# Optimization experiments

Hardware: AMD Instinct MI355X
Metric: run time of the kernel (lower is better)

## Reference

```python
import jax, jax.numpy as jnp
import numpy as np

MAX_REL = 64  # max_relative_position (init kwarg)


def setup_inputs() -> dict:
    B, S, D, K = 8, 2048, 256, MAX_REL
    key = jax.random.key(0)
    ks = jax.random.split(key, 12)
    scale = 0.02
    return {
        "repre": jax.random.normal(ks[0], (B, S, D), jnp.float32),
        "mask": jnp.ones((B, S), jnp.int32),
        "wq1": jax.random.normal(ks[1], (D, D), jnp.float32) * scale,
        "bq1": jnp.zeros((D,), jnp.float32),
        "wk1": jax.random.normal(ks[2], (D, D), jnp.float32) * scale,
        "bk1": jnp.zeros((D,), jnp.float32),
        "rel1": jax.random.normal(ks[3], (2 * K + 1, D), jnp.float32) * scale,
        "wq2": jax.random.normal(ks[4], (D, D), jnp.float32) * scale,
        "bq2": jnp.zeros((D,), jnp.float32),
        "wk2": jax.random.normal(ks[5], (D, D), jnp.float32) * scale,
        "bk2": jnp.zeros((D,), jnp.float32),
        "rel2": jax.random.normal(ks[6], (2 * K + 1, D), jnp.float32) * scale,
    }


def _attn_logits(x, wq, bq, wk, bk, rel_emb, invalid, rel_idx):
    # Single-head relative-position attention scores (OpenNMT style):
    # query is pre-scaled by 1/sqrt(d); relative-key bias folded into scores.
    B, S, D = x.shape
    q = (x @ wq.T + bq) / jnp.sqrt(jnp.asarray(D, x.dtype))  # [B,S,D]
    k = x @ wk.T + bk                                        # [B,S,D]
    scores = jnp.einsum("bqd,bkd->bqk", q, k)               # [B,S,S]
    # relative-position term: q . rel_emb[clip(k-q)] without the [S,S,D] table
    q_rel = jnp.einsum("bqd,rd->bqr", q, rel_emb)            # [B,S,2K+1]
    idx = jnp.broadcast_to(rel_idx[None, :, :], (B, S, S))
    rel_scores = jnp.take_along_axis(q_rel, idx, axis=2)     # [B,S,S]
    scores = scores + rel_scores
    return jnp.where(invalid, jnp.asarray(-1e18, scores.dtype), scores)


def reference(repre, mask, wq1, bq1, wk1, bk1, rel1, wq2, bq2, wk2, bk2, rel2):
    B, S, D = repre.shape
    K = MAX_REL
    pos = jnp.arange(S)
    rel_idx = jnp.clip(pos[None, :] - pos[:, None], -K, K) + K  # [S,S] in [0,2K]
    # square_mask = ~(mask^T @ mask): attend only where both positions valid
    invalid = (mask[:, :, None] * mask[:, None, :]) == 0        # [B,S,S] bool
    span_st_logits = _attn_logits(repre, wq1, bq1, wk1, bk1, rel1, invalid, rel_idx)
    span_ed_logits = _attn_logits(repre, wq2, bq2, wk2, bk2, rel2, invalid, rel_idx)
    return (span_st_logits, span_ed_logits)
```

## Files before the change

### kernel.cpp

```cpp
#include <hip/hip_runtime.h>
#include <hip/hip_bf16.h>

typedef __attribute__((ext_vector_type(4))) float f32x4;
typedef __attribute__((ext_vector_type(8))) short short8;

struct bf16x4 { __hip_bfloat16 a, b, c, d; };

#define BS   8
#define SQ   2048
#define DD   256
#define KREL 64
#define NREL 129

static const size_t OFF_XBF   = 0;
static const size_t OFF_WBF   = 8388608;
static const size_t OFF_RELBF = 8912896;
static const size_t OFF_WR    = 9044992;
static const size_t OFF_CR    = 9307136;
static const size_t OFF_QK    = 9309184;
static const size_t OFF_QR    = 42863616;

struct ConvArgs {
  const float* src[7];
  __hip_bfloat16* dst[7];
  float scale[7];
  int cum4[8];
};
struct bf4 { __hip_bfloat16 a, b, c, d; };

__global__ __launch_bounds__(256) void convert_k(ConvArgs A) {
  const int idx = blockIdx.x * 256 + threadIdx.x;
  if (idx >= A.cum4[7]) return;
  int rg = 0;
  #pragma unroll
  for (int t = 1; t < 7; ++t) rg += (idx >= A.cum4[t]);
  const int local = idx - A.cum4[rg];
  const float4 v = ((const float4*)A.src[rg])[local];
  const float sc = A.scale[rg];
  bf4 o;
  o.a = __float2bfloat16(v.x * sc);
  o.b = __float2bfloat16(v.y * sc);
  o.c = __float2bfloat16(v.z * sc);
  o.d = __float2bfloat16(v.w * sc);
  ((bf4*)A.dst[rg])[local] = o;
}

__global__ __launch_bounds__(256) void wr_k(const __hip_bfloat16* __restrict__ relbf,
                                            const __hip_bfloat16* __restrict__ wbf,
                                            const float* __restrict__ bq1,
                                            const float* __restrict__ bq2,
                                            __hip_bfloat16* __restrict__ wr,
                                            float* __restrict__ cr) {
  const int r = blockIdx.x;
  const int h = blockIdx.y;
  const int e = threadIdx.x;
  const int lane = e & 63, wv = e >> 6;
  const __hip_bfloat16* rel = relbf + (size_t)h * (NREL * DD);
  const __hip_bfloat16* wq  = wbf + (size_t)h * (2 * DD * DD);
  float a0 = 0.f, a1 = 0.f, a2 = 0.f, a3 = 0.f;
  if (r < NREL) {
    #pragma unroll 4
    for (int d = 0; d < DD; d += 4) {
      a0 += __bfloat162float(rel[r * DD + d + 0]) * __bfloat162float(wq[(d + 0) * DD + e]);
      a1 += __bfloat162float(rel[r * DD + d + 1]) * __bfloat162float(wq[(d + 1) * DD + e]);
      a2 += __bfloat162float(rel[r * DD + d + 2]) * __bfloat162float(wq[(d + 2) * DD + e]);
      a3 += __bfloat162float(rel[r * DD + d + 3]) * __bfloat162float(wq[(d + 3) * DD + e]);
    }
  }
  wr[((size_t)h * DD + r) * DD + e] = __float2bfloat16((a0 + a1) + (a2 + a3));

  const float* bq = h ? bq2 : bq1;
  float p = (r < NREL) ? bq[e] * 0.0625f * __bfloat162float(rel[r * DD + e]) : 0.f;
  #pragma unroll
  for (int o = 32; o > 0; o >>= 1) p += __shfl_down(p, o, 64);
  __shared__ float wred[4];
  if (lane == 0) wred[wv] = p;
  __syncthreads();
  if (e == 0) cr[h * DD + r] = (wred[0] + wred[1]) + (wred[2] + wred[3]);
}

__device__ __forceinline__ void stage_tile(const __hip_bfloat16* __restrict__ A,
                                           const __hip_bfloat16* __restrict__ B,
                                           int rowBase, int colBase, int k0,
                                           char* As, char* Bs, int wv, int lane) {
  #pragma unroll
  for (int inst = 0; inst < 2; ++inst) {
    const int lds_off = wv * 2048 + inst * 1024;
    const int e0 = (lds_off >> 1) + lane * 8;
    const int r  = e0 >> 5;
    const int kk = e0 & 31;
    __builtin_amdgcn_global_load_lds(
        (const __attribute__((address_space(1))) void*)(A + (size_t)(rowBase + r) * DD + k0 + kk),
        (__attribute__((address_space(3))) void*)(As + lds_off), 16, 0, 0);
    __builtin_amdgcn_global_load_lds(
        (const __attribute__((address_space(1))) void*)(B + (size_t)(colBase + r) * DD + k0 + kk),
        (__attribute__((address_space(3))) void*)(Bs + lds_off), 16, 0, 0);
  }
}

__device__ __forceinline__ void gemm_dbuf(const __hip_bfloat16* __restrict__ A,
                                          const __hip_bfloat16* __restrict__ B,
                                          int rowBase, int colBase,
                                          char* lds,
                                          f32x4 acc[4][4]) {
  const int tid  = threadIdx.x;
  const int lane = tid & 63;
  const int wv   = tid >> 6;
  const int wrow = (wv >> 1) * 64;
  const int wcol = (wv & 1) * 64;
  const int m    = lane & 15;
  const int quad = lane >> 4;

  char* As[2] = {lds, lds + 16384};
  char* Bs[2] = {lds + 8192, lds + 24576};

  const f32x4 zf = {0.f, 0.f, 0.f, 0.f};
  #pragma unroll
  for (int si = 0; si < 4; ++si)
    #pragma unroll
    for (int sj = 0; sj < 4; ++sj) acc[si][sj] = zf;

  stage_tile(A, B, rowBase, colBase, 0, As[0], Bs[0], wv, lane);
  __syncthreads();

  #pragma unroll
  for (int k = 0; k < 8; ++k) {
    const int cur = k & 1, nxt = cur ^ 1;
    if (k < 7)
      stage_tile(A, B, rowBase, colBase, (k + 1) * 32, As[nxt], Bs[nxt], wv, lane);

    short8 af[4], bf[4];
    #pragma unroll
    for (int s = 0; s < 4; ++s) {
      af[s] = *(const short8*)(As[cur] + (wrow + s * 16 + m) * 64 + quad * 16);
      bf[s] = *(const short8*)(Bs[cur] + (wcol + s * 16 + m) * 64 + quad * 16);
    }
    #pragma unroll
    for (int si = 0; si < 4; ++si)
      #pragma unroll
      for (int sj = 0; sj < 4; ++sj)
        acc[si][sj] = __builtin_amdgcn_mfma_f32_16x16x32_bf16(bf[sj], af[si], acc[si][sj], 0, 0, 0);
    __syncthreads();
  }
}

struct QKArgs {
  const __hip_bfloat16* X;
  const __hip_bfloat16* W[6];
  const float* bias[6];
  void* out[6];
  float bscale[6];
  int isf32[6];
};

__global__ __launch_bounds__(256) void qk_k(QKArgs A) {
  __shared__ char lds[32768];
  const int flat = blockIdx.x + (blockIdx.y << 1) + (blockIdx.z << 8);
  const int swz  = (flat & 7) * 192 + (flat >> 3);
  const int colT = swz & 1;
  const int rowT = (swz >> 1) & 127;
  const int z    = swz >> 8;
  const int rowBase = rowT * 128;
  const int colBase = colT * 128;
  f32x4 acc[4][4];
  gemm_dbuf(A.X, A.W[z], rowBase, colBase, lds, acc);

  const int tid  = threadIdx.x;
  const int lane = tid & 63;
  const int wv   = tid >> 6;
  const int wrow = (wv >> 1) * 64;
  const int wcol = (wv & 1) * 64;
  const int m    = lane & 15;
  const int quad = lane >> 4;

  const float* bias = A.bias[z];
  const float bs = A.bscale[z];
  const int f32o = A.isf32[z];
  float* fo = (float*)A.out[z];
  __hip_bfloat16* bo = (__hip_bfloat16*)A.out[z];

  #pragma unroll
  for (int si = 0; si < 4; ++si) {
    const int i = rowBase + wrow + si * 16 + m;
    #pragma unroll
    for (int sj = 0; sj < 4; ++sj) {
      const int j0 = colBase + wcol + sj * 16 + quad * 4;
      const f32x4 bj = *(const f32x4*)(bias + j0);
      f32x4 v;
      #pragma unroll
      for (int r = 0; r < 4; ++r) v[r] = acc[si][sj][r] + bj[r] * bs;
      const size_t idx = (size_t)i * DD + j0;
      if (f32o) {
        __builtin_nontemporal_store(v, (f32x4*)(fo + idx));
      } else {
        bf16x4 o;
        o.a = __float2bfloat16(v[0]);
        o.b = __float2bfloat16(v[1]);
        o.c = __float2bfloat16(v[2]);
        o.d = __float2bfloat16(v[3]);
        unsigned long long u;
        __builtin_memcpy(&u, &o, 8);
        __builtin_nontemporal_store(u, (unsigned long long*)(bo + idx));
      }
    }
  }
}

__global__ __launch_bounds__(256) void score_k(const __hip_bfloat16* __restrict__ Q1,
                                               const __hip_bfloat16* __restrict__ K1,
                                               const float* __restrict__ QR1,
                                               const __hip_bfloat16* __restrict__ Q2,
                                               const __hip_bfloat16* __restrict__ K2,
                                               const float* __restrict__ QR2,
                                               const int* __restrict__ mask,
                                               float* __restrict__ out) {
  __shared__ char lds[32768];
  const int flat = blockIdx.x + (blockIdx.y << 4) + (blockIdx.z << 8);
  const int swz  = ((flat & 7) << 9) | (flat >> 3);
  const int colT = swz & 15;
  const int rowT = (swz >> 4) & 15;
  const int z    = swz >> 8;
  const int h = z >> 3, b = z & 7;
  const __hip_bfloat16* Q  = (h ? Q2 : Q1) + (size_t)b * SQ * DD;
  const __hip_bfloat16* Kk = (h ? K2 : K1) + (size_t)b * SQ * DD;
  const float* QR = (h ? QR2 : QR1) + (size_t)b * SQ * DD;
  const int* mk = mask + b * SQ;
  float* outp = out + (size_t)z * SQ * SQ;
  const int rowBase = rowT * 128;
  const int colBase = colT * 128;

  f32x4 acc[4][4];
  gemm_dbuf(Q, Kk, rowBase, colBase, lds, acc);

  const int tid  = threadIdx.x;
  const int lane = tid & 63;
  const int wv   = tid >> 6;
  const int wrow = (wv >> 1) * 64;
  const int wcol = (wv & 1) * 64;
  const int m    = lane & 15;
  const int quad = lane >> 4;

  const int delta = colBase - rowBase;
  const int mode = (delta >= 192) ? 1 : (delta <= -192 ? -1 : 0);

  int4 mj4[4];
  #pragma unroll
  for (int sj = 0; sj < 4; ++sj)
    mj4[sj] = *(const int4*)(mk + colBase + wcol + sj * 16 + quad * 4);

  #pragma unroll
  for (int si = 0; si < 4; ++si) {
    const int i = rowBase + wrow + si * 16 + m;
    const int mi = mk[i];
    const float* qr_row = QR + (size_t)i * DD;
    float* orow = outp + (size_t)i * SQ;
    float relc = 0.f;
    if (mode) relc = qr_row[mode == 1 ? 2 * KREL : 0];
    #pragma unroll
    for (int sj = 0; sj < 4; ++sj) {
      const int j0 = colBase + wcol + sj * 16 + quad * 4;
      f32x4 v;
      if (mode) {
        #pragma unroll
        for (int r = 0; r < 4; ++r) v[r] = acc[si][sj][r] + relc;
      } else {
        #pragma unroll
        for (int r = 0; r < 4; ++r) {
          int d = j0 + r - i;
          d = d < -KREL ? -KREL : (d > KREL ? KREL : d);
          v[r] = acc[si][sj][r] + qr_row[d + KREL];
        }
      }
      const int4 mj = mj4[sj];
      if (!(mi && mj.x)) v[0] = -1e18f;
      if (!(mi && mj.y)) v[1] = -1e18f;
      if (!(mi && mj.z)) v[2] = -1e18f;
      if (!(mi && mj.w)) v[3] = -1e18f;
      __builtin_nontemporal_store(v, (f32x4*)(orow + j0));
    }
  }
}

extern "C" void kernel_launch(void* const* d_in, const int* in_sizes, int n_in,
                              void* d_out, int out_size, void* d_ws, size_t ws_size,
                              hipStream_t stream) {
  const float* repre = (const float*)d_in[0];
  const int*   mask  = (const int*)d_in[1];
  const float* wq1 = (const float*)d_in[2];
  const float* bq1 = (const float*)d_in[3];
  const float* wk1 = (const float*)d_in[4];
  const float* bk1 = (const float*)d_in[5];
  const float* rel1 = (const float*)d_in[6];
  const float* wq2 = (const float*)d_in[7];
  const float* bq2 = (const float*)d_in[8];
  const float* wk2 = (const float*)d_in[9];
  const float* bk2 = (const float*)d_in[10];
  const float* rel2 = (const float*)d_in[11];

  char* ws = (char*)d_ws;
  __hip_bfloat16* xbf   = (__hip_bfloat16*)(ws + OFF_XBF);
  __hip_bfloat16* wbf   = (__hip_bfloat16*)(ws + OFF_WBF);
  __hip_bfloat16* relbf = (__hip_bfloat16*)(ws + OFF_RELBF);
  __hip_bfloat16* wr    = (__hip_bfloat16*)(ws + OFF_WR);
  float*          cr    = (float*)(ws + OFF_CR);
  __hip_bfloat16* Q1 = (__hip_bfloat16*)(ws + OFF_QK);
  __hip_bfloat16* K1 = Q1 + (size_t)16384 * 256;
  __hip_bfloat16* Q2 = K1 + (size_t)16384 * 256;
  __hip_bfloat16* K2 = Q2 + (size_t)16384 * 256;
  float* QR1 = (float*)(ws + OFF_QR);
  float* QR2 = QR1 + (size_t)16384 * 256;

  ConvArgs ca;
  ca.src[0] = repre; ca.dst[0] = xbf;            ca.scale[0] = 1.f;
  ca.src[1] = wq1;   ca.dst[1] = wbf;            ca.scale[1] = 0.0625f;
  ca.src[2] = wk1;   ca.dst[2] = wbf + 65536;    ca.scale[2] = 1.f;
  ca.src[3] = wq2;   ca.dst[3] = wbf + 131072;   ca.scale[3] = 0.0625f;
  ca.src[4] = wk2;   ca.dst[4] = wbf + 196608;   ca.scale[4] = 1.f;
  ca.src[5] = rel1;  ca.dst[5] = relbf;          ca.scale[5] = 1.f;
  ca.src[6] = rel2;  ca.dst[6] = relbf + 33024;  ca.scale[6] = 1.f;
  const int sizes[7] = {4194304, 65536, 65536, 65536, 65536, 33024, 33024};
  int cum = 0;
  ca.cum4[0] = 0;
  for (int i = 0; i < 7; ++i) { cum += sizes[i] / 4; ca.cum4[i + 1] = cum; }
  const int nblk = (cum + 255) / 256;
  hipLaunchKernelGGL(convert_k, dim3(nblk), dim3(256), 0, stream, ca);

  hipLaunchKernelGGL(wr_k, dim3(256, 2), dim3(256), 0, stream, relbf, wbf, bq1, bq2, wr, cr);

  QKArgs qa;
  qa.X = xbf;
  qa.W[0] = wbf;          qa.bias[0] = bq1;      qa.bscale[0] = 0.0625f; qa.out[0] = Q1;  qa.isf32[0] = 0;
  qa.W[1] = wbf + 65536;  qa.bias[1] = bk1;      qa.bscale[1] = 1.f;     qa.out[1] = K1;  qa.isf32[1] = 0;
  qa.W[2] = wr;           qa.bias[2] = cr;       qa.bscale[2] = 1.f;     qa.out[2] = QR1; qa.isf32[2] = 1;
  qa.W[3] = wbf + 131072; qa.bias[3] = bq2;      qa.bscale[3] = 0.0625f; qa.out[3] = Q2;  qa.isf32[3] = 0;
  qa.W[4] = wbf + 196608; qa.bias[4] = bk2;      qa.bscale[4] = 1.f;     qa.out[4] = K2;  qa.isf32[4] = 0;
  qa.W[5] = wr + 65536;   qa.bias[5] = cr + 256; qa.bscale[5] = 1.f;     qa.out[5] = QR2; qa.isf32[5] = 1;
  hipLaunchKernelGGL(qk_k, dim3(2, 128, 6), dim3(256), 0, stream, qa);

  hipLaunchKernelGGL(score_k, dim3(16, 16, 16), dim3(256), 0, stream,
                     Q1, K1, QR1, Q2, K2, QR2, mask, (float*)d_out);
}
```

Before: 488.4 us.

## Triple-buffer GEMM K-loop with single barrier and use regular stores

```diff
diff --git a/kernel.cpp b/kernel.cpp
--- a/kernel.cpp
+++ b/kernel.cpp
@@ -98,7 +98,7 @@
   }
 }
 
-__device__ __forceinline__ void gemm_dbuf(const __hip_bfloat16* __restrict__ A,
+__device__ __forceinline__ void gemm_tbuf(const __hip_bfloat16* __restrict__ A,
                                           const __hip_bfloat16* __restrict__ B,
                                           int rowBase, int colBase,
                                           char* lds,
@@ -111,8 +111,8 @@
   const int m    = lane & 15;
   const int quad = lane >> 4;
 
-  char* As[2] = {lds, lds + 16384};
-  char* Bs[2] = {lds + 8192, lds + 24576};
+  char* As[3] = {lds,        lds + 16384, lds + 32768};
+  char* Bs[3] = {lds + 8192, lds + 24576, lds + 40960};
 
   const f32x4 zf = {0.f, 0.f, 0.f, 0.f};
   #pragma unroll
@@ -120,15 +120,21 @@
     #pragma unroll
     for (int sj = 0; sj < 4; ++sj) acc[si][sj] = zf;
 
-  stage_tile(A, B, rowBase, colBase, 0, As[0], Bs[0], wv, lane);
-  __syncthreads();
+  stage_tile(A, B, rowBase, colBase, 0,  As[0], Bs[0], wv, lane);
+  stage_tile(A, B, rowBase, colBase, 32, As[1], Bs[1], wv, lane);
 
   #pragma unroll
   for (int k = 0; k < 8; ++k) {
-    const int cur = k & 1, nxt = cur ^ 1;
-    if (k < 7)
-      stage_tile(A, B, rowBase, colBase, (k + 1) * 32, As[nxt], Bs[nxt], wv, lane);
-
+    if (k < 7) asm volatile("s_waitcnt vmcnt(4)" ::: "memory");
+    else       asm volatile("s_waitcnt vmcnt(0)" ::: "memory");
+    __builtin_amdgcn_sched_barrier(0);
+    __builtin_amdgcn_s_barrier();
+    __builtin_amdgcn_sched_barrier(0);
+    if (k < 6)
+      stage_tile(A, B, rowBase, colBase, (k + 2) * 32,
+                 As[(k + 2) % 3], Bs[(k + 2) % 3], wv, lane);
+
+    const int cur = k % 3;
     short8 af[4], bf[4];
     #pragma unroll
     for (int s = 0; s < 4; ++s) {
@@ -140,7 +146,6 @@
       #pragma unroll
       for (int sj = 0; sj < 4; ++sj)
         acc[si][sj] = __builtin_amdgcn_mfma_f32_16x16x32_bf16(bf[sj], af[si], acc[si][sj], 0, 0, 0);
-    __syncthreads();
   }
 }
 
@@ -154,7 +159,7 @@
 };
 
 __global__ __launch_bounds__(256) void qk_k(QKArgs A) {
-  __shared__ char lds[32768];
+  __shared__ char lds[49152];
   const int flat = blockIdx.x + (blockIdx.y << 1) + (blockIdx.z << 8);
   const int swz  = (flat & 7) * 192 + (flat >> 3);
   const int colT = swz & 1;
@@ -163,7 +168,7 @@
   const int rowBase = rowT * 128;
   const int colBase = colT * 128;
   f32x4 acc[4][4];
-  gemm_dbuf(A.X, A.W[z], rowBase, colBase, lds, acc);
+  gemm_tbuf(A.X, A.W[z], rowBase, colBase, lds, acc);
 
   const int tid  = threadIdx.x;
   const int lane = tid & 63;
@@ -191,16 +196,14 @@
       for (int r = 0; r < 4; ++r) v[r] = acc[si][sj][r] + bj[r] * bs;
       const size_t idx = (size_t)i * DD + j0;
       if (f32o) {
-        __builtin_nontemporal_store(v, (f32x4*)(fo + idx));
+        *(f32x4*)(fo + idx) = v;
       } else {
         bf16x4 o;
         o.a = __float2bfloat16(v[0]);
         o.b = __float2bfloat16(v[1]);
         o.c = __float2bfloat16(v[2]);
         o.d = __float2bfloat16(v[3]);
-        unsigned long long u;
-        __builtin_memcpy(&u, &o, 8);
-        __builtin_nontemporal_store(u, (unsigned long long*)(bo + idx));
+        *(bf16x4*)(bo + idx) = o;
       }
     }
   }
@@ -214,7 +217,7 @@
                                                const float* __restrict__ QR2,
                                                const int* __restrict__ mask,
                                                float* __restrict__ out) {
-  __shared__ char lds[32768];
+  __shared__ char lds[49152];
   const int flat = blockIdx.x + (blockIdx.y << 4) + (blockIdx.z << 8);
   const int swz  = ((flat & 7) << 9) | (flat >> 3);
   const int colT = swz & 15;
@@ -230,7 +233,7 @@
   const int colBase = colT * 128;
 
   f32x4 acc[4][4];
-  gemm_dbuf(Q, Kk, rowBase, colBase, lds, acc);
+  gemm_tbuf(Q, Kk, rowBase, colBase, lds, acc);
 
   const int tid  = threadIdx.x;
   const int lane = tid & 63;
@@ -276,7 +279,7 @@
       if (!(mi && mj.y)) v[1] = -1e18f;
       if (!(mi && mj.z)) v[2] = -1e18f;
       if (!(mi && mj.w)) v[3] = -1e18f;
-      __builtin_nontemporal_store(v, (f32x4*)(orow + j0));
+      *(f32x4*)(orow + j0) = v;
     }
   }
 }
```

Measured after the change: 405.0 us. 17.1% less time.
